# Optimization experiments

Hardware: AMD Instinct MI355X
Metric: run time of the kernel (lower is better)

The kernel has to match this reference:

```python
import jax, jax.numpy as jnp
import numpy as np

N_SEG = 16384      # number of ragged segments (customers)
SEG_LEN = 1024     # events per segment (uniform here; math supports ragged)
N = N_SEG * SEG_LEN
EPS = 1e-5


def setup_inputs() -> dict:
    key = jax.random.key(0)
    k1, k2 = jax.random.split(key)
    # tau = detached model prediction of next inter-event time; must be > 0
    tau = jax.random.uniform(k1, (N,), jnp.float32, 0.1, 2.0)
    # dt = observed inter-event times (non-negative)
    dt = jax.random.uniform(k2, (N,), jnp.float32, 0.0, 1.0)
    # offsets: B+1 boundaries of the ragged segments within the flat arrays
    offsets = jnp.arange(N_SEG + 1, dtype=jnp.int32) * SEG_LEN
    return {"tau": tau, "dt": dt, "offsets": offsets}


def reference(tau, dt, offsets):
    # Original loop: per segment, drop first and last event, accumulate
    # -log_prob under Exponential(rate=1/tau):
    #   -log_prob(x) = log(tau) + (dt + eps) / tau
    # Replaced by a single masked elementwise pass + sum: interior mask is
    # everything except each segment's first index and last index.
    n = dt.shape[0]
    mask = (
        jnp.ones((n,), dtype=bool)
        .at[offsets[:-1]].set(False)      # segment starts
        .at[offsets[1:] - 1].set(False)   # segment ends
    )
    tau_sg = jax.lax.stop_gradient(tau)   # y_pred['next_dt'].detach()
    nll = jnp.log(tau_sg) + (dt + EPS) / tau_sg
    loss = jnp.sum(jnp.where(mask, nll, jnp.zeros((), nll.dtype)))
    final_loss = loss / offsets.shape[0]  # divide by B+1, as in source
    return final_loss
```

## Files before the change

### kernel.cpp

```cpp
#include <hip/hip_runtime.h>

#define EPS 1e-5f
#define THREADS 256
#define MAIN_BLOCKS 2048
#define SUPER 2048
#define BND_THREADS 256

__global__ __launch_bounds__(THREADS, 4) void tau_loss_main(
    const float4* __restrict__ t4,
    const float4* __restrict__ d4,
    const float* __restrict__ tau,
    const float* __restrict__ dt,
    float* __restrict__ ws,
    int n) {
    const int n4 = n >> 2;
    const int nsuper = n4 / SUPER;

    float a0 = 0.f, a1 = 0.f, a2 = 0.f, a3 = 0.f;

    for (int s = blockIdx.x; s < nsuper; s += MAIN_BLOCKS) {
        const int base = s * SUPER + (int)threadIdx.x;
        float4 t0 = t4[base + 0 * THREADS];
        float4 t1 = t4[base + 1 * THREADS];
        float4 t2 = t4[base + 2 * THREADS];
        float4 t3 = t4[base + 3 * THREADS];
        float4 t4v = t4[base + 4 * THREADS];
        float4 t5 = t4[base + 5 * THREADS];
        float4 t6 = t4[base + 6 * THREADS];
        float4 t7 = t4[base + 7 * THREADS];
        float4 e0 = d4[base + 0 * THREADS];
        float4 e1 = d4[base + 1 * THREADS];
        float4 e2 = d4[base + 2 * THREADS];
        float4 e3 = d4[base + 3 * THREADS];
        float4 e4 = d4[base + 4 * THREADS];
        float4 e5 = d4[base + 5 * THREADS];
        float4 e6 = d4[base + 6 * THREADS];
        float4 e7 = d4[base + 7 * THREADS];
        a0 += __logf(t0.x) + __fdividef(e0.x + EPS, t0.x);
        a1 += __logf(t0.y) + __fdividef(e0.y + EPS, t0.y);
        a2 += __logf(t0.z) + __fdividef(e0.z + EPS, t0.z);
        a3 += __logf(t0.w) + __fdividef(e0.w + EPS, t0.w);
        a0 += __logf(t1.x) + __fdividef(e1.x + EPS, t1.x);
        a1 += __logf(t1.y) + __fdividef(e1.y + EPS, t1.y);
        a2 += __logf(t1.z) + __fdividef(e1.z + EPS, t1.z);
        a3 += __logf(t1.w) + __fdividef(e1.w + EPS, t1.w);
        a0 += __logf(t2.x) + __fdividef(e2.x + EPS, t2.x);
        a1 += __logf(t2.y) + __fdividef(e2.y + EPS, t2.y);
        a2 += __logf(t2.z) + __fdividef(e2.z + EPS, t2.z);
        a3 += __logf(t2.w) + __fdividef(e2.w + EPS, t2.w);
        a0 += __logf(t3.x) + __fdividef(e3.x + EPS, t3.x);
        a1 += __logf(t3.y) + __fdividef(e3.y + EPS, t3.y);
        a2 += __logf(t3.z) + __fdividef(e3.z + EPS, t3.z);
        a3 += __logf(t3.w) + __fdividef(e3.w + EPS, t3.w);
        a0 += __logf(t4v.x) + __fdividef(e4.x + EPS, t4v.x);
        a1 += __logf(t4v.y) + __fdividef(e4.y + EPS, t4v.y);
        a2 += __logf(t4v.z) + __fdividef(e4.z + EPS, t4v.z);
        a3 += __logf(t4v.w) + __fdividef(e4.w + EPS, t4v.w);
        a0 += __logf(t5.x) + __fdividef(e5.x + EPS, t5.x);
        a1 += __logf(t5.y) + __fdividef(e5.y + EPS, t5.y);
        a2 += __logf(t5.z) + __fdividef(e5.z + EPS, t5.z);
        a3 += __logf(t5.w) + __fdividef(e5.w + EPS, t5.w);
        a0 += __logf(t6.x) + __fdividef(e6.x + EPS, t6.x);
        a1 += __logf(t6.y) + __fdividef(e6.y + EPS, t6.y);
        a2 += __logf(t6.z) + __fdividef(e6.z + EPS, t6.z);
        a3 += __logf(t6.w) + __fdividef(e6.w + EPS, t6.w);
        a0 += __logf(t7.x) + __fdividef(e7.x + EPS, t7.x);
        a1 += __logf(t7.y) + __fdividef(e7.y + EPS, t7.y);
        a2 += __logf(t7.z) + __fdividef(e7.z + EPS, t7.z);
        a3 += __logf(t7.w) + __fdividef(e7.w + EPS, t7.w);
    }

    if (blockIdx.x == 0) {
        for (int i = nsuper * (SUPER * 4) + (int)threadIdx.x; i < n; i += THREADS) {
            float t = tau[i];
            a0 += __logf(t) + __fdividef(dt[i] + EPS, t);
        }
    }

    float acc = (a0 + a1) + (a2 + a3);

    #pragma unroll
    for (int off = 32; off > 0; off >>= 1)
        acc += __shfl_down(acc, off, 64);

    __shared__ float smem[THREADS / 64];
    int wave = threadIdx.x >> 6;
    int lane = threadIdx.x & 63;
    if (lane == 0) smem[wave] = acc;
    __syncthreads();
    if (threadIdx.x == 0)
        ws[blockIdx.x] = smem[0] + smem[1] + smem[2] + smem[3];
}

__global__ __launch_bounds__(BND_THREADS) void tau_loss_boundary(
    const float* __restrict__ tau,
    const float* __restrict__ dt,
    const int* __restrict__ offsets,
    float* __restrict__ ws,
    int nseg) {
    int k = blockIdx.x * blockDim.x + threadIdx.x;

    float sub = 0.0f;
    if (k < nseg) {
        int s = offsets[k];
        int e = offsets[k + 1] - 1;
        float ts = tau[s];
        sub = __logf(ts) + __fdividef(dt[s] + EPS, ts);
        if (e != s) {
            float te = tau[e];
            sub += __logf(te) + __fdividef(dt[e] + EPS, te);
        }
    }

    #pragma unroll
    for (int off = 32; off > 0; off >>= 1)
        sub += __shfl_down(sub, off, 64);

    __shared__ float smem[BND_THREADS / 64];
    int wave = threadIdx.x >> 6;
    int lane = threadIdx.x & 63;
    if (lane == 0) smem[wave] = sub;
    __syncthreads();
    if (threadIdx.x == 0)
        ws[MAIN_BLOCKS + blockIdx.x] = -(smem[0] + smem[1] + smem[2] + smem[3]);
}

__global__ __launch_bounds__(256) void tau_loss_final(
    const float* __restrict__ ws, int m, float inv_div,
    float* __restrict__ out) {
    float a = 0.f;
    for (int i = threadIdx.x; i < m; i += 256)
        a += ws[i];

    #pragma unroll
    for (int off = 32; off > 0; off >>= 1)
        a += __shfl_down(a, off, 64);

    __shared__ float smem[4];
    int wave = threadIdx.x >> 6;
    int lane = threadIdx.x & 63;
    if (lane == 0) smem[wave] = a;
    __syncthreads();
    if (threadIdx.x == 0)
        out[0] = (smem[0] + smem[1] + smem[2] + smem[3]) * inv_div;
}

extern "C" void kernel_launch(void* const* d_in, const int* in_sizes, int n_in,
                              void* d_out, int out_size, void* d_ws, size_t ws_size,
                              hipStream_t stream) {
    const float* tau = (const float*)d_in[0];
    const float* dt  = (const float*)d_in[1];
    const int* offsets = (const int*)d_in[2];
    float* out = (float*)d_out;
    float* ws = (float*)d_ws;

    const int n = in_sizes[0];
    const int n_off = in_sizes[2];
    const int nseg = n_off - 1;
    const float inv_div = 1.0f / (float)n_off;

    tau_loss_main<<<MAIN_BLOCKS, THREADS, 0, stream>>>(
        (const float4*)tau, (const float4*)dt, tau, dt, ws, n);

    int bblocks = (nseg + BND_THREADS - 1) / BND_THREADS;
    if (bblocks < 1) bblocks = 1;
    tau_loss_boundary<<<bblocks, BND_THREADS, 0, stream>>>(tau, dt, offsets, ws, nseg);

    tau_loss_final<<<1, 256, 0, stream>>>(ws, MAIN_BLOCKS + bblocks, inv_div, out);
}
```

Before: 35.76 us.

## Fuse main, boundary and final reduction kernels into one with last-block reduction

```diff
diff --git a/kernel.cpp b/kernel.cpp
--- a/kernel.cpp
+++ b/kernel.cpp
@@ -4,145 +4,152 @@
 #define THREADS 256
 #define MAIN_BLOCKS 2048
 #define SUPER 2048
-#define BND_THREADS 256
 
-__global__ __launch_bounds__(THREADS, 4) void tau_loss_main(
+__global__ __launch_bounds__(THREADS, 4) void tau_loss_fused(
     const float4* __restrict__ t4,
     const float4* __restrict__ d4,
     const float* __restrict__ tau,
     const float* __restrict__ dt,
-    float* __restrict__ ws,
-    int n) {
-    const int n4 = n >> 2;
-    const int nsuper = n4 / SUPER;
-
-    float a0 = 0.f, a1 = 0.f, a2 = 0.f, a3 = 0.f;
-
-    for (int s = blockIdx.x; s < nsuper; s += MAIN_BLOCKS) {
-        const int base = s * SUPER + (int)threadIdx.x;
-        float4 t0 = t4[base + 0 * THREADS];
-        float4 t1 = t4[base + 1 * THREADS];
-        float4 t2 = t4[base + 2 * THREADS];
-        float4 t3 = t4[base + 3 * THREADS];
-        float4 t4v = t4[base + 4 * THREADS];
-        float4 t5 = t4[base + 5 * THREADS];
-        float4 t6 = t4[base + 6 * THREADS];
-        float4 t7 = t4[base + 7 * THREADS];
-        float4 e0 = d4[base + 0 * THREADS];
-        float4 e1 = d4[base + 1 * THREADS];
-        float4 e2 = d4[base + 2 * THREADS];
-        float4 e3 = d4[base + 3 * THREADS];
-        float4 e4 = d4[base + 4 * THREADS];
-        float4 e5 = d4[base + 5 * THREADS];
-        float4 e6 = d4[base + 6 * THREADS];
-        float4 e7 = d4[base + 7 * THREADS];
-        a0 += __logf(t0.x) + __fdividef(e0.x + EPS, t0.x);
-        a1 += __logf(t0.y) + __fdividef(e0.y + EPS, t0.y);
-        a2 += __logf(t0.z) + __fdividef(e0.z + EPS, t0.z);
-        a3 += __logf(t0.w) + __fdividef(e0.w + EPS, t0.w);
-        a0 += __logf(t1.x) + __fdividef(e1.x + EPS, t1.x);
-        a1 += __logf(t1.y) + __fdividef(e1.y + EPS, t1.y);
-        a2 += __logf(t1.z) + __fdividef(e1.z + EPS, t1.z);
-        a3 += __logf(t1.w) + __fdividef(e1.w + EPS, t1.w);
-        a0 += __logf(t2.x) + __fdividef(e2.x + EPS, t2.x);
-        a1 += __logf(t2.y) + __fdividef(e2.y + EPS, t2.y);
-        a2 += __logf(t2.z) + __fdividef(e2.z + EPS, t2.z);
-        a3 += __logf(t2.w) + __fdividef(e2.w + EPS, t2.w);
-        a0 += __logf(t3.x) + __fdividef(e3.x + EPS, t3.x);
-        a1 += __logf(t3.y) + __fdividef(e3.y + EPS, t3.y);
-        a2 += __logf(t3.z) + __fdividef(e3.z + EPS, t3.z);
-        a3 += __logf(t3.w) + __fdividef(e3.w + EPS, t3.w);
-        a0 += __logf(t4v.x) + __fdividef(e4.x + EPS, t4v.x);
-        a1 += __logf(t4v.y) + __fdividef(e4.y + EPS, t4v.y);
-        a2 += __logf(t4v.z) + __fdividef(e4.z + EPS, t4v.z);
-        a3 += __logf(t4v.w) + __fdividef(e4.w + EPS, t4v.w);
-        a0 += __logf(t5.x) + __fdividef(e5.x + EPS, t5.x);
-        a1 += __logf(t5.y) + __fdividef(e5.y + EPS, t5.y);
-        a2 += __logf(t5.z) + __fdividef(e5.z + EPS, t5.z);
-        a3 += __logf(t5.w) + __fdividef(e5.w + EPS, t5.w);
-        a0 += __logf(t6.x) + __fdividef(e6.x + EPS, t6.x);
-        a1 += __logf(t6.y) + __fdividef(e6.y + EPS, t6.y);
-        a2 += __logf(t6.z) + __fdividef(e6.z + EPS, t6.z);
-        a3 += __logf(t6.w) + __fdividef(e6.w + EPS, t6.w);
-        a0 += __logf(t7.x) + __fdividef(e7.x + EPS, t7.x);
-        a1 += __logf(t7.y) + __fdividef(e7.y + EPS, t7.y);
-        a2 += __logf(t7.z) + __fdividef(e7.z + EPS, t7.z);
-        a3 += __logf(t7.w) + __fdividef(e7.w + EPS, t7.w);
-    }
-
-    if (blockIdx.x == 0) {
-        for (int i = nsuper * (SUPER * 4) + (int)threadIdx.x; i < n; i += THREADS) {
-            float t = tau[i];
-            a0 += __logf(t) + __fdividef(dt[i] + EPS, t);
-        }
-    }
-
-    float acc = (a0 + a1) + (a2 + a3);
-
-    #pragma unroll
-    for (int off = 32; off > 0; off >>= 1)
-        acc += __shfl_down(acc, off, 64);
-
-    __shared__ float smem[THREADS / 64];
-    int wave = threadIdx.x >> 6;
-    int lane = threadIdx.x & 63;
-    if (lane == 0) smem[wave] = acc;
-    __syncthreads();
-    if (threadIdx.x == 0)
-        ws[blockIdx.x] = smem[0] + smem[1] + smem[2] + smem[3];
-}
-
-__global__ __launch_bounds__(BND_THREADS) void tau_loss_boundary(
-    const float* __restrict__ tau,
-    const float* __restrict__ dt,
     const int* __restrict__ offsets,
     float* __restrict__ ws,
-    int nseg) {
-    int k = blockIdx.x * blockDim.x + threadIdx.x;
+    int* __restrict__ counter,
+    int n, int nseg, int nBnd, float inv_div,
+    float* __restrict__ out) {
 
-    float sub = 0.0f;
-    if (k < nseg) {
-        int s = offsets[k];
-        int e = offsets[k + 1] - 1;
-        float ts = tau[s];
-        sub = __logf(ts) + __fdividef(dt[s] + EPS, ts);
-        if (e != s) {
-            float te = tau[e];
-            sub += __logf(te) + __fdividef(dt[e] + EPS, te);
+    float partial = 0.0f;
+
+    if ((int)blockIdx.x < nBnd) {
+        int k = blockIdx.x * THREADS + threadIdx.x;
+        float sub = 0.0f;
+        if (k < nseg) {
+            int s = offsets[k];
+            int e = offsets[k + 1] - 1;
+            float ts = tau[s];
+            sub = __logf(ts) + __fdividef(dt[s] + EPS, ts);
+            if (e != s) {
+                float te = tau[e];
+                sub += __logf(te) + __fdividef(dt[e] + EPS, te);
+            }
         }
+        partial = -sub;
+    } else {
+        const int mb = (int)blockIdx.x - nBnd;
+        const int n4 = n >> 2;
+        const int nsuper = n4 / SUPER;
+
+        float a0 = 0.f, a1 = 0.f, a2 = 0.f, a3 = 0.f;
+
+        for (int s = mb; s < nsuper; s += MAIN_BLOCKS) {
+            const int base = s * SUPER + (int)threadIdx.x;
+            float4 t0 = t4[base + 0 * THREADS];
+            float4 t1 = t4[base + 1 * THREADS];
+            float4 t2 = t4[base + 2 * THREADS];
+            float4 t3 = t4[base + 3 * THREADS];
+            float4 t4v = t4[base + 4 * THREADS];
+            float4 t5 = t4[base + 5 * THREADS];
+            float4 t6 = t4[base + 6 * THREADS];
+            float4 t7 = t4[base + 7 * THREADS];
+            float4 e0 = d4[base + 0 * THREADS];
+            float4 e1 = d4[base + 1 * THREADS];
+            float4 e2 = d4[base + 2 * THREADS];
+            float4 e3 = d4[base + 3 * THREADS];
+            float4 e4 = d4[base + 4 * THREADS];
+            float4 e5 = d4[base + 5 * THREADS];
+            float4 e6 = d4[base + 6 * THREADS];
+            float4 e7 = d4[base + 7 * THREADS];
+            a0 += __logf(t0.x) + __fdividef(e0.x + EPS, t0.x);
+            a1 += __logf(t0.y) + __fdividef(e0.y + EPS, t0.y);
+            a2 += __logf(t0.z) + __fdividef(e0.z + EPS, t0.z);
+            a3 += __logf(t0.w) + __fdividef(e0.w + EPS, t0.w);
+            a0 += __logf(t1.x) + __fdividef(e1.x + EPS, t1.x);
+            a1 += __logf(t1.y) + __fdividef(e1.y + EPS, t1.y);
+            a2 += __logf(t1.z) + __fdividef(e1.z + EPS, t1.z);
+            a3 += __logf(t1.w) + __fdividef(e1.w + EPS, t1.w);
+            a0 += __logf(t2.x) + __fdividef(e2.x + EPS, t2.x);
+            a1 += __logf(t2.y) + __fdividef(e2.y + EPS, t2.y);
+            a2 += __logf(t2.z) + __fdividef(e2.z + EPS, t2.z);
+            a3 += __logf(t2.w) + __fdividef(e2.w + EPS, t2.w);
+            a0 += __logf(t3.x) + __fdividef(e3.x + EPS, t3.x);
+            a1 += __logf(t3.y) + __fdividef(e3.y + EPS, t3.y);
+            a2 += __logf(t3.z) + __fdividef(e3.z + EPS, t3.z);
+            a3 += __logf(t3.w) + __fdividef(e3.w + EPS, t3.w);
+            a0 += __logf(t4v.x) + __fdividef(e4.x + EPS, t4v.x);
+            a1 += __logf(t4v.y) + __fdividef(e4.y + EPS, t4v.y);
+            a2 += __logf(t4v.z) + __fdividef(e4.z + EPS, t4v.z);
+            a3 += __logf(t4v.w) + __fdividef(e4.w + EPS, t4v.w);
+            a0 += __logf(t5.x) + __fdividef(e5.x + EPS, t5.x);
+            a1 += __logf(t5.y) + __fdividef(e5.y + EPS, t5.y);
+            a2 += __logf(t5.z) + __fdividef(e5.z + EPS, t5.z);
+            a3 += __logf(t5.w) + __fdividef(e5.w + EPS, t5.w);
+            a0 += __logf(t6.x) + __fdividef(e6.x + EPS, t6.x);
+            a1 += __logf(t6.y) + __fdividef(e6.y + EPS, t6.y);
+            a2 += __logf(t6.z) + __fdividef(e6.z + EPS, t6.z);
+            a3 += __logf(t6.w) + __fdividef(e6.w + EPS, t6.w);
+            a0 += __logf(t7.x) + __fdividef(e7.x + EPS, t7.x);
+            a1 += __logf(t7.y) + __fdividef(e7.y + EPS, t7.y);
+            a2 += __logf(t7.z) + __fdividef(e7.z + EPS, t7.z);
+            a3 += __logf(t7.w) + __fdividef(e7.w + EPS, t7.w);
+        }
+
+        if (mb == 0) {
+            for (int i = nsuper * (SUPER * 4) + (int)threadIdx.x; i < n; i += THREADS) {
+                float t = tau[i];
+                a0 += __logf(t) + __fdividef(dt[i] + EPS, t);
+            }
+        }
+        partial = (a0 + a1) + (a2 + a3);
     }
 
     #pragma unroll
     for (int off = 32; off > 0; off >>= 1)
-        sub += __shfl_down(sub, off, 64);
+        partial += __shfl_down(partial, off, 64);
 
-    __shared__ float smem[BND_THREADS / 64];
+    __shared__ float smem[THREADS / 64];
+    __shared__ int flag;
     int wave = threadIdx.x >> 6;
     int lane = threadIdx.x & 63;
-    if (lane == 0) smem[wave] = sub;
+    if (lane == 0) smem[wave] = partial;
     __syncthreads();
-    if (threadIdx.x == 0)
-        ws[MAIN_BLOCKS + blockIdx.x] = -(smem[0] + smem[1] + smem[2] + smem[3]);
-}
 
-__global__ __launch_bounds__(256) void tau_loss_final(
-    const float* __restrict__ ws, int m, float inv_div,
-    float* __restrict__ out) {
-    float a = 0.f;
-    for (int i = threadIdx.x; i < m; i += 256)
-        a += ws[i];
+    if (threadIdx.x == 0) {
+        float p = smem[0] + smem[1] + smem[2] + smem[3];
+        __hip_atomic_store(&ws[blockIdx.x], p, __ATOMIC_RELAXED,
+                           __HIP_MEMORY_SCOPE_AGENT);
+        int old = __hip_atomic_fetch_add(counter, 1, __ATOMIC_ACQ_REL,
+                                         __HIP_MEMORY_SCOPE_AGENT);
+        flag = (old == (int)gridDim.x - 1) ? 1 : 0;
+    }
+    __syncthreads();
 
-    #pragma unroll
-    for (int off = 32; off > 0; off >>= 1)
-        a += __shfl_down(a, off, 64);
+    if (flag) {
+        const int total = (int)gridDim.x;
+        float b0 = 0.f, b1 = 0.f, b2 = 0.f, b3 = 0.f;
+        int i = (int)threadIdx.x;
+        for (; i + 3 * THREADS < total; i += 4 * THREADS) {
+            b0 += __hip_atomic_load(&ws[i + 0 * THREADS], __ATOMIC_RELAXED,
+                                    __HIP_MEMORY_SCOPE_AGENT);
+            b1 += __hip_atomic_load(&ws[i + 1 * THREADS], __ATOMIC_RELAXED,
+                                    __HIP_MEMORY_SCOPE_AGENT);
+            b2 += __hip_atomic_load(&ws[i + 2 * THREADS], __ATOMIC_RELAXED,
+                                    __HIP_MEMORY_SCOPE_AGENT);
+            b3 += __hip_atomic_load(&ws[i + 3 * THREADS], __ATOMIC_RELAXED,
+                                    __HIP_MEMORY_SCOPE_AGENT);
+        }
+        for (; i < total; i += THREADS)
+            b0 += __hip_atomic_load(&ws[i], __ATOMIC_RELAXED,
+                                    __HIP_MEMORY_SCOPE_AGENT);
+        float a = (b0 + b1) + (b2 + b3);
 
-    __shared__ float smem[4];
-    int wave = threadIdx.x >> 6;
-    int lane = threadIdx.x & 63;
-    if (lane == 0) smem[wave] = a;
-    __syncthreads();
-    if (threadIdx.x == 0)
-        out[0] = (smem[0] + smem[1] + smem[2] + smem[3]) * inv_div;
+        #pragma unroll
+        for (int off = 32; off > 0; off >>= 1)
+            a += __shfl_down(a, off, 64);
+
+        __shared__ float smem2[THREADS / 64];
+        if (lane == 0) smem2[wave] = a;
+        __syncthreads();
+        if (threadIdx.x == 0)
+            out[0] = (smem2[0] + smem2[1] + smem2[2] + smem2[3]) * inv_div;
+    }
 }
 
 extern "C" void kernel_launch(void* const* d_in, const int* in_sizes, int n_in,
@@ -159,12 +166,14 @@
     const int nseg = n_off - 1;
     const float inv_div = 1.0f / (float)n_off;
 
-    tau_loss_main<<<MAIN_BLOCKS, THREADS, 0, stream>>>(
-        (const float4*)tau, (const float4*)dt, tau, dt, ws, n);
+    int nBnd = (nseg + THREADS - 1) / THREADS;
+    if (nBnd < 1) nBnd = 1;
+    const int grid = nBnd + MAIN_BLOCKS;
+    int* counter = (int*)(ws + grid);
 
-    int bblocks = (nseg + BND_THREADS - 1) / BND_THREADS;
-    if (bblocks < 1) bblocks = 1;
-    tau_loss_boundary<<<bblocks, BND_THREADS, 0, stream>>>(tau, dt, offsets, ws, nseg);
+    hipMemsetAsync(counter, 0, sizeof(int), stream);
 
-    tau_loss_final<<<1, 256, 0, stream>>>(ws, MAIN_BLOCKS + bblocks, inv_div, out);
+    tau_loss_fused<<<grid, THREADS, 0, stream>>>(
+        (const float4*)tau, (const float4*)dt, tau, dt, offsets,
+        ws, counter, n, nseg, nBnd, inv_div, out);
 }
```

New measurement: 95.26 us. +166.4%, slower.
